# Optimization experiments

Hardware: AMD Instinct MI355X
Metric: run time of the kernel (lower is better)

The kernel has to match this reference:

```python
import jax, jax.numpy as jnp
import numpy as np

EPS = 1e-5
GN_GROUPS = 4  # ConvBlock groupnorm num_groups

def _conv3d(x, w, b):
    # x: [B,C,D,H,W], w: [O,I,3,3,3]
    y = jax.lax.conv_general_dilated(x, w, (1, 1, 1), 'SAME',
                                     dimension_numbers=('NCDHW', 'OIDHW', 'NCDHW'))
    return y + b[None, :, None, None, None]

def _groupnorm(x, gamma, beta):
    b, c, d, h, w = x.shape
    xg = x.reshape(b, GN_GROUPS, c // GN_GROUPS, d, h, w)
    m = xg.mean(axis=(2, 3, 4, 5), keepdims=True)
    v = xg.var(axis=(2, 3, 4, 5), keepdims=True)
    xn = ((xg - m) * jax.lax.rsqrt(v + EPS)).reshape(b, c, d, h, w)
    return xn * gamma[None, :, None, None, None] + beta[None, :, None, None, None]

def setup_inputs() -> dict:
    key = jax.random.key(0)
    ks = jax.random.split(key, 8)
    B, C, D, H, W = 4, 64, 16, 16, 16
    R = 4
    f = lambda k, s: jax.random.normal(k, s, dtype=jnp.float32) * 0.05
    return {
        'x': jax.random.normal(ks[0], (B, C, D, H, W), dtype=jnp.float32),
        'w_i': f(ks[1], (C, C, 3, 3, 3)), 'b_i': jnp.zeros((C,), jnp.float32),
        'gamma_i': jnp.ones((C,), jnp.float32), 'beta_i': jnp.zeros((C,), jnp.float32),
        'w_q': f(ks[2], (C // R, C)), 'b_q': jnp.zeros((C // R,), jnp.float32),
        'w_k': f(ks[3], (C // R, C)), 'b_k': jnp.zeros((C // R,), jnp.float32),
        'w_v': f(ks[4], (C, C)), 'b_v': jnp.zeros((C,), jnp.float32),
        'w_o': f(ks[5], (C, C, 3, 3, 3)), 'b_o': jnp.zeros((C,), jnp.float32),
        'gamma_o': jnp.ones((C,), jnp.float32), 'beta_o': jnp.zeros((C,), jnp.float32),
    }

def reference(x, w_i, b_i, gamma_i, beta_i, w_q, b_q, w_k, b_k, w_v, b_v,
              w_o, b_o, gamma_o, beta_o):
    # i_conv: Conv3d(3x3x3) -> GroupNorm(4) -> ReLU
    x = jax.nn.relu(_groupnorm(_conv3d(x, w_i, b_i), gamma_i, beta_i))
    b, c, d, h, w = x.shape
    n = d * h * w
    xf = x.reshape(b, c, n)
    # spatial attention (groups=1): conv1x1 projections as channel matmuls
    q = jnp.einsum('oc,bcn->bon', w_q, xf) + b_q[None, :, None]   # [b, c/r, n]
    k = jnp.einsum('oc,bcn->bon', w_k, xf) + b_k[None, :, None]   # [b, c/r, n]
    v = jnp.einsum('oc,bcn->bon', w_v, xf) + b_v[None, :, None]   # [b, c,   n]
    A = jax.nn.softmax(jnp.einsum('bqn,bqm->bnm', q, k), axis=-1)  # [b, n, n]
    # ans = bmm(value, A^T): ans[b,c,m] = sum_n v[b,c,n] * A[b,m,n]
    sa = jnp.einsum('bcn,bmn->bcm', v, A).reshape(b, c, d, h, w)
    # channel attention
    Ac = jax.nn.softmax(jnp.einsum('bcn,bdn->bcd', xf, xf), axis=-1)  # [b, c, c]
    ca = jnp.einsum('bcd,bdn->bcn', Ac, xf).reshape(b, c, d, h, w)
    y = x + sa + ca
    # o_conv
    return jax.nn.relu(_groupnorm(_conv3d(y, w_o, b_o), gamma_o, beta_o))
```

## Files before the change

### kernel.cpp

```cpp
#include <hip/hip_runtime.h>

#define OFF_T0  0
#define OFF_SA  1048576
#define OFF_QT  2097152
#define OFF_KT  2359296
#define OFF_VB  2621440
#define OFF_YT  3145728
#define OFF_XB  3670016
#define OFF_AC  4194304
#define OFF_WBI 4210688
#define OFF_WBO 4265984
#define OFF_PT  4321280
#define OFF_PO  4325376
#define OFF_MS  6422528
#define WS_NEED ((size_t)6553600 * 4)

typedef __attribute__((ext_vector_type(8))) short short8v;
typedef __attribute__((ext_vector_type(4))) short short4v;
typedef __attribute__((ext_vector_type(4))) float f32x4;

__device__ __forceinline__ ushort f2bf(float f) {
  union { float f; unsigned u; } v; v.f = f;
  unsigned r = (v.u + 0x7fffu + ((v.u >> 16) & 1u)) >> 16;
  return (ushort)r;
}
__device__ __forceinline__ float bf2f(ushort u) {
  union { unsigned u; float f; } v; v.u = ((unsigned)u) << 16;
  return v.f;
}

__global__ __launch_bounds__(256) void wcvt2_k(const float* __restrict__ wi, const float* __restrict__ wo,
    ushort* __restrict__ wbi, ushort* __restrict__ wbo) {
  int idx = blockIdx.x * 256 + threadIdx.x;
  const float* w = idx < 110592 ? wi : wo;
  ushort* wb = idx < 110592 ? wbi : wbo;
  int j = idx < 110592 ? idx : idx - 110592;
  int ci = j & 63, tap = (j >> 6) % 27, co = j / (64 * 27);
  wb[j] = f2bf(w[(co * 64 + ci) * 27 + tap]);
}

__global__ __launch_bounds__(256) void xcvt_k(const float* __restrict__ x, ushort* __restrict__ xb,
    float* __restrict__ pt) {
  if (blockIdx.x == 0 && threadIdx.x < 64) pt[threadIdx.x] = 0.f;
  __shared__ ushort tl[64 * 72];
  int b = blockIdx.x >> 6;
  int n0 = (blockIdx.x & 63) * 64;
  int t = threadIdx.x;
  int ci = t >> 2, q = t & 3;
  const float* src = x + (size_t)(b * 64 + ci) * 4096 + n0 + q * 16;
  #pragma unroll
  for (int i = 0; i < 4; ++i) {
    float4 v = *reinterpret_cast<const float4*>(src + i * 4);
    tl[(q * 16 + i * 4 + 0) * 72 + ci] = f2bf(v.x);
    tl[(q * 16 + i * 4 + 1) * 72 + ci] = f2bf(v.y);
    tl[(q * 16 + i * 4 + 2) * 72 + ci] = f2bf(v.z);
    tl[(q * 16 + i * 4 + 3) * 72 + ci] = f2bf(v.w);
  }
  __syncthreads();
  int n = t >> 2, qq = t & 3;
  ushort* dst = xb + (size_t)(b * 4096 + n0 + n) * 64 + qq * 16;
  *reinterpret_cast<short8v*>(dst) = *reinterpret_cast<const short8v*>(&tl[n * 72 + qq * 16]);
  *reinterpret_cast<short8v*>(dst + 8) = *reinterpret_cast<const short8v*>(&tl[n * 72 + qq * 16 + 8]);
}

__global__ __launch_bounds__(256) void conv_mfma_k(const ushort* __restrict__ xt,
    const ushort* __restrict__ wb, const float* __restrict__ bias, float* __restrict__ out,
    float* __restrict__ ptg) {
  __shared__ __align__(16) ushort xls[18 * 18 * 64];
  __shared__ float sh_st[16];
  int blk = blockIdx.x;
  int h0 = (blk & 3) * 4;
  int d0 = (blk >> 2) & 15;
  int b  = blk >> 6;
  int tid = threadIdx.x;

  const ushort* xtb = xt + (size_t)b * 4096 * 64;
  for (int u = tid; u < 324; u += 256) {
    int w_s = u % 18;
    int row = u / 18;
    int dz = row / 6, h_s = row - dz * 6;
    int d = d0 + dz - 1, h = h0 + h_s - 1, w = w_s - 1;
    ushort* dst = &xls[(row * 18 + w_s) * 64];
    int swz = w_s & 7;
    if (d >= 0 && d < 16 && h >= 0 && h < 16 && w >= 0 && w < 16) {
      const ushort* src = xtb + (size_t)(d * 256 + h * 16 + w) * 64;
      #pragma unroll
      for (int c = 0; c < 8; ++c)
        *reinterpret_cast<short8v*>(dst + ((c ^ swz) << 3)) =
            *reinterpret_cast<const short8v*>(src + (c << 3));
    } else {
      short8v z = {};
      #pragma unroll
      for (int c = 0; c < 8; ++c)
        *reinterpret_cast<short8v*>(dst + ((c ^ swz) << 3)) = z;
    }
  }
  __syncthreads();

  int wv = tid >> 6, l = tid & 63;
  int wn = wv >> 1, wc = wv & 1;
  int lm = l & 15, lg = l >> 4;

  f32x4 acc[2][2] = {};
  const ushort* wbase0 = wb + (size_t)((wc * 2 + 0) * 16 + lm) * 1728 + lg * 8;
  const ushort* wbase1 = wb + (size_t)((wc * 2 + 1) * 16 + lm) * 1728 + lg * 8;

  #pragma unroll 6
  for (int s = 0; s < 54; ++s) {
    int tap = s >> 1, c0h = s & 1;
    int dz = tap / 9, dyx = tap - dz * 9;
    int dy = dyx / 3, dx = dyx - dy * 3;
    int wrow = lm + dx;
    int chunk = ((c0h * 4 + lg) ^ (wrow & 7)) << 3;
    int r0 = ((dz * 6 + wn * 2 + dy) * 18 + wrow) * 64 + chunk;
    short8v a0 = *reinterpret_cast<const short8v*>(&xls[r0]);
    short8v a1 = *reinterpret_cast<const short8v*>(&xls[r0 + 18 * 64]);
    short8v b0 = *reinterpret_cast<const short8v*>(wbase0 + s * 32);
    short8v b1 = *reinterpret_cast<const short8v*>(wbase1 + s * 32);
    acc[0][0] = __builtin_amdgcn_mfma_f32_16x16x32_bf16(a0, b0, acc[0][0], 0, 0, 0);
    acc[0][1] = __builtin_amdgcn_mfma_f32_16x16x32_bf16(a0, b1, acc[0][1], 0, 0, 0);
    acc[1][0] = __builtin_amdgcn_mfma_f32_16x16x32_bf16(a1, b0, acc[1][0], 0, 0, 0);
    acc[1][1] = __builtin_amdgcn_mfma_f32_16x16x32_bf16(a1, b1, acc[1][1], 0, 0, 0);
  }

  float gs[2], gss[2];
  #pragma unroll
  for (int j = 0; j < 2; ++j) {
    gs[j] = 0.f; gss[j] = 0.f;
    int co = (wc * 2 + j) * 16 + lm;
    float bs = bias[co];
    #pragma unroll
    for (int i = 0; i < 2; ++i) {
      int hh = h0 + wn * 2 + i;
      float4 o;
      o.x = acc[i][j][0] + bs; o.y = acc[i][j][1] + bs;
      o.z = acc[i][j][2] + bs; o.w = acc[i][j][3] + bs;
      gs[j]  += o.x + o.y + o.z + o.w;
      gss[j] = fmaf(o.x, o.x, gss[j]); gss[j] = fmaf(o.y, o.y, gss[j]);
      gss[j] = fmaf(o.z, o.z, gss[j]); gss[j] = fmaf(o.w, o.w, gss[j]);
      *reinterpret_cast<float4*>(&out[(size_t)(b * 64 + co) * 4096 + d0 * 256 + hh * 16 + lg * 4]) = o;
    }
  }
  #pragma unroll
  for (int j = 0; j < 2; ++j) {
    #pragma unroll
    for (int off = 32; off > 0; off >>= 1) {
      gs[j]  += __shfl_xor(gs[j], off);
      gss[j] += __shfl_xor(gss[j], off);
    }
    if (l == 0) { sh_st[wv * 4 + j * 2] = gs[j]; sh_st[wv * 4 + j * 2 + 1] = gss[j]; }
  }
  __syncthreads();
  if (tid < 8) {
    int g = tid >> 1, w2 = tid & 1;
    int wcg = g >> 1, j = g & 1;
    float v = sh_st[wcg * 4 + j * 2 + w2] + sh_st[(wcg + 2) * 4 + j * 2 + w2];
    atomicAdd(&ptg[(b * 4 + g) * 2 + w2], v);
  }
}

__global__ __launch_bounds__(256) void gn_apply_k(const float* __restrict__ t, const float* __restrict__ pt,
    const float* __restrict__ gamma, const float* __restrict__ beta, float* __restrict__ out) {
  int idx = blockIdx.x * 256 + threadIdx.x;
  int c = (idx >> 12) & 63, b = idx >> 18;
  int bg = b * 4 + (c >> 4);
  float s0 = pt[bg * 2], ss0 = pt[bg * 2 + 1];
  float m = s0 * (1.f / 65536.f);
  float r = rsqrtf(ss0 * (1.f / 65536.f) - m * m + 1e-5f);
  float ga = r * gamma[c], bb2 = beta[c] - m * r * gamma[c];
  out[idx] = fmaxf(fmaf(t[idx], ga, bb2), 0.f);
}

__global__ __launch_bounds__(256) void proj_all_k(const float* __restrict__ t0, const float* __restrict__ pt0,
    const float* __restrict__ gamma, const float* __restrict__ beta,
    const float* __restrict__ wq, const float* __restrict__ bq,
    const float* __restrict__ wk, const float* __restrict__ bk,
    const float* __restrict__ wv_, const float* __restrict__ bv,
    ushort* __restrict__ qt, ushort* __restrict__ kt, ushort* __restrict__ vt) {
  __shared__ float xls[64 * 68];
  int b = blockIdx.x >> 6, n0 = (blockIdx.x & 63) * 64;
  int tid = threadIdx.x;
  {
    int ci = tid >> 2, q = tid & 3;
    int bg = b * 4 + (ci >> 4);
    float s0 = pt0[bg * 2], ss0 = pt0[bg * 2 + 1];
    float m = s0 * (1.f / 65536.f);
    float rv = rsqrtf(ss0 * (1.f / 65536.f) - m * m + 1e-5f);
    float ga = rv * gamma[ci], bb2 = beta[ci] - m * rv * gamma[ci];
    const float* src = t0 + (size_t)(b * 64 + ci) * 4096 + n0 + q * 16;
    #pragma unroll
    for (int i = 0; i < 4; ++i) {
      float4 v = *reinterpret_cast<const float4*>(src + i * 4);
      float* d = &xls[ci * 68 + q * 16 + i * 4];
      d[0] = fmaxf(fmaf(v.x, ga, bb2), 0.f);
      d[1] = fmaxf(fmaf(v.y, ga, bb2), 0.f);
      d[2] = fmaxf(fmaf(v.z, ga, bb2), 0.f);
      d[3] = fmaxf(fmaf(v.w, ga, bb2), 0.f);
    }
  }
  __syncthreads();
  int n = tid & 63, og = tid >> 6;
  float xr[64];
  #pragma unroll
  for (int c = 0; c < 64; ++c) xr[c] = xls[c * 68 + n];
  if (og < 2) {
    const float* w  = og == 0 ? wq : wk;
    const float* bb = og == 0 ? bq : bk;
    float scale = og == 0 ? 1.4426950408889634f : 1.0f;
    ushort* outp = og == 0 ? qt : kt;
    union { ushort u[16]; short8v v[2]; } pk;
    #pragma unroll
    for (int o = 0; o < 16; ++o) {
      const float* wr = w + o * 64;
      float acc = bb[o];
      #pragma unroll
      for (int c = 0; c < 64; ++c) acc = fmaf(wr[c], xr[c], acc);
      pk.u[o] = f2bf(acc * scale);
    }
    ushort* dst = outp + (size_t)(b * 4096 + n0 + n) * 32;
    *reinterpret_cast<short8v*>(dst) = pk.v[0];
    *reinterpret_cast<short8v*>(dst + 8) = pk.v[1];
    short8v z = {};
    *reinterpret_cast<short8v*>(dst + 16) = z;
    *reinterpret_cast<short8v*>(dst + 24) = z;
  } else {
    int o0 = (og - 2) * 32;
    #pragma unroll
    for (int o = 0; o < 32; ++o) {
      const float* wr = wv_ + (o0 + o) * 64;
      float acc = bv[o0 + o];
      #pragma unroll
      for (int c = 0; c < 64; ++c) acc = fmaf(wr[c], xr[c], acc);
      vt[(size_t)(b * 64 + o0 + o) * 4096 + n0 + n] = f2bf(acc);
    }
  }
}

#define KP 40
#define VP 72
template<bool SPLIT>
__global__ __launch_bounds__(256) void flash_mfma_k(const ushort* __restrict__ qt,
    const ushort* __restrict__ kt, const ushort* __restrict__ vb, float* __restrict__ sa,
    ushort* __restrict__ pacc, float* __restrict__ pms) {
  __shared__ __align__(16) ushort kls[2][64 * KP];
  __shared__ __align__(16) ushort vls[2][64 * VP];
  __shared__ __align__(16) ushort pls[64 * VP];
  int s, mt, b;
  if (SPLIT) { s = blockIdx.x & 3; mt = (blockIdx.x >> 2) & 63; b = blockIdx.x >> 8; }
  else       { s = 0; mt = blockIdx.x & 63; b = blockIdx.x >> 6; }
  const int NT = SPLIT ? 16 : 64;
  int m0 = mt * 64;
  int kofs = s * 1024;
  int tid = threadIdx.x;
  int w = tid >> 6, l = tid & 63;
  int lm = l & 15, lg = l >> 4;

  short8v qf = *reinterpret_cast<const short8v*>(
      qt + (size_t)(b * 4096 + m0 + w * 16 + lm) * 32 + lg * 8);

  f32x4 acc[4] = {};
  float M = -1e30f, S = 0.f;

  int sr = tid >> 2, sq = tid & 3;
  const ushort* ksrc = kt + (size_t)b * 4096 * 32 + (size_t)kofs * 32 + (size_t)sr * 32 + sq * 8;
  const ushort* vsrc = vb + (size_t)b * 64 * 4096 + (size_t)sr * 4096 + kofs + sq * 16;
  int koff = sr * KP + sq * 8;
  int voff = sr * VP + sq * 16;

  {
    short8v kr = *reinterpret_cast<const short8v*>(ksrc);
    short8v v0 = *reinterpret_cast<const short8v*>(vsrc);
    short8v v1 = *reinterpret_cast<const short8v*>(vsrc + 8);
    *reinterpret_cast<short8v*>(&kls[0][koff]) = kr;
    *reinterpret_cast<short8v*>(&vls[0][voff]) = v0;
    *reinterpret_cast<short8v*>(&vls[0][voff + 8]) = v1;
  }

  ushort* plb = &pls[(w * 16 + lm) * VP];

  #pragma unroll 2
  for (int it = 0; it < NT; ++it) {
    int cur = it & 1;
    int nx = it < NT - 1 ? it + 1 : NT - 1;
    short8v knr = *reinterpret_cast<const short8v*>(ksrc + (size_t)nx * 2048);
    short8v vn0 = *reinterpret_cast<const short8v*>(vsrc + nx * 64);
    short8v vn1 = *reinterpret_cast<const short8v*>(vsrc + nx * 64 + 8);

    __syncthreads();

    const ushort* kb  = &kls[cur][0];
    const ushort* vbk = &vls[cur][0];

    f32x4 sf[4];
    #pragma unroll
    for (int nt = 0; nt < 4; ++nt) {
      short8v kf = *reinterpret_cast<const short8v*>(&kb[(nt * 16 + lm) * KP + lg * 8]);
      f32x4 z = {};
      sf[nt] = __builtin_amdgcn_mfma_f32_16x16x32_bf16(kf, qf, z, 0, 0, 0);
    }

    float tmax = -1e30f;
    #pragma unroll
    for (int nt = 0; nt < 4; ++nt)
      #pragma unroll
      for (int r = 0; r < 4; ++r) tmax = fmaxf(tmax, sf[nt][r]);
    tmax = fmaxf(tmax, __shfl_xor(tmax, 16));
    tmax = fmaxf(tmax, __shfl_xor(tmax, 32));
    if (!__all(tmax <= M)) {
      float Mn = fmaxf(M, tmax);
      float sc = __builtin_amdgcn_exp2f(M - Mn);
      M = Mn;
      S *= sc;
      #pragma unroll
      for (int ct = 0; ct < 4; ++ct)
        #pragma unroll
        for (int r = 0; r < 4; ++r) acc[ct][r] *= sc;
    }
    float tsum = 0.f;
    float p[16];
    #pragma unroll
    for (int nt = 0; nt < 4; ++nt)
      #pragma unroll
      for (int r = 0; r < 4; ++r) {
        float e = __builtin_amdgcn_exp2f(sf[nt][r] - M);
        p[nt * 4 + r] = e;
        tsum += e;
      }
    tsum += __shfl_xor(tsum, 16);
    tsum += __shfl_xor(tsum, 32);
    S += tsum;

    #pragma unroll
    for (int nt = 0; nt < 4; ++nt) {
      unsigned p01, p23;
      asm("v_cvt_pk_bf16_f32 %0, %1, %2" : "=v"(p01) : "v"(p[nt * 4 + 0]), "v"(p[nt * 4 + 1]));
      asm("v_cvt_pk_bf16_f32 %0, %1, %2" : "=v"(p23) : "v"(p[nt * 4 + 2]), "v"(p[nt * 4 + 3]));
      union { unsigned u[2]; short4v v; } pk;
      pk.u[0] = p01; pk.u[1] = p23;
      *reinterpret_cast<short4v*>(plb + nt * 16 + lg * 4) = pk.v;
    }
    asm volatile("s_waitcnt lgkmcnt(0)" ::: "memory");
    __builtin_amdgcn_sched_barrier(0);

    #pragma unroll
    for (int nh = 0; nh < 2; ++nh) {
      short8v pf = *reinterpret_cast<const short8v*>(plb + nh * 32 + lg * 8);
      #pragma unroll
      for (int ct = 0; ct < 4; ++ct) {
        short8v vf = *reinterpret_cast<const short8v*>(&vbk[(ct * 16 + lm) * VP + nh * 32 + lg * 8]);
        acc[ct] = __builtin_amdgcn_mfma_f32_16x16x32_bf16(vf, pf, acc[ct], 0, 0, 0);
      }
    }

    if (it < NT - 1) {
      *reinterpret_cast<short8v*>(&kls[cur ^ 1][koff]) = knr;
      *reinterpret_cast<short8v*>(&vls[cur ^ 1][voff]) = vn0;
      *reinterpret_cast<short8v*>(&vls[cur ^ 1][voff + 8]) = vn1;
    }
  }

  if (SPLIT) {
    int blk = (b * 64 + mt) * 4 + s;
    ushort* pa = pacc + (size_t)blk * 4096;
    #pragma unroll
    for (int ct = 0; ct < 4; ++ct)
      #pragma unroll
      for (int r = 0; r < 4; ++r)
        pa[(ct * 16 + lg * 4 + r) * 64 + w * 16 + lm] = f2bf(acc[ct][r]);
    if (l < 16) {
      pms[(size_t)blk * 128 + (w * 16 + lm) * 2]     = M;
      pms[(size_t)blk * 128 + (w * 16 + lm) * 2 + 1] = S;
    }
  } else {
    float inv = 1.f / S;
    #pragma unroll
    for (int ct = 0; ct < 4; ++ct)
      #pragma unroll
      for (int r = 0; r < 4; ++r)
        sa[(size_t)(b * 64 + ct * 16 + lg * 4 + r) * 4096 + m0 + w * 16 + lm] = acc[ct][r] * inv;
  }
}

__global__ __launch_bounds__(256) void gram_partial_k(const float* __restrict__ t0,
    const float* __restrict__ pt0, const float* __restrict__ gamma, const float* __restrict__ beta,
    float* __restrict__ pg) {
  __shared__ __align__(16) ushort hi[64 * 64];
  __shared__ __align__(16) ushort lo[64 * 64];
  int b = blockIdx.x >> 5, ks = blockIdx.x & 31;
  int tid = threadIdx.x;
  int wv = tid >> 6, l = tid & 63, lm = l & 15, lg = l >> 4;
  int wr = wv >> 1, wd = wv & 1;
  f32x4 acc[2][2] = {};
  int sr = tid >> 2, sq = tid & 3;
  int bg = b * 4 + (sr >> 4);
  float s0p = pt0[bg * 2], ss0p = pt0[bg * 2 + 1];
  float mq = s0p * (1.f / 65536.f);
  float rq = rsqrtf(ss0p * (1.f / 65536.f) - mq * mq + 1e-5f);
  float ga = rq * gamma[sr], bb2 = beta[sr] - mq * rq * gamma[sr];
  const float* xb = t0 + (size_t)b * 262144;

  for (int kt = 0; kt < 2; ++kt) {
    int n0 = ks * 128 + kt * 64;
    __syncthreads();
    const float* src = xb + (size_t)sr * 4096 + n0 + sq * 16;
    #pragma unroll
    for (int c2 = 0; c2 < 2; ++c2) {
      int chunk = sq * 2 + c2;
      int dchunk = chunk ^ (sr & 7);
      short8v hvv, lvv;
      #pragma unroll
      for (int j = 0; j < 8; ++j) {
        float v = fmaxf(fmaf(src[c2 * 8 + j], ga, bb2), 0.f);
        ushort hb = f2bf(v);
        union { float f; unsigned u; } uu; uu.u = ((unsigned)hb) << 16;
        hvv[j] = (short)hb;
        lvv[j] = (short)f2bf(v - uu.f);
      }
      *reinterpret_cast<short8v*>(&hi[sr * 64 + dchunk * 8]) = hvv;
      *reinterpret_cast<short8v*>(&lo[sr * 64 + dchunk * 8]) = lvv;
    }
    __syncthreads();
    #pragma unroll
    for (int kk = 0; kk < 2; ++kk) {
      short8v ah[2], al[2], bh[2], bl[2];
      #pragma unroll
      for (int i = 0; i < 2; ++i) {
        int rc = wr * 32 + i * 16 + lm;
        int ca = ((kk * 4 + lg) ^ (rc & 7)) * 8;
        ah[i] = *reinterpret_cast<const short8v*>(&hi[rc * 64 + ca]);
        al[i] = *reinterpret_cast<const short8v*>(&lo[rc * 64 + ca]);
        int rd = wd * 32 + i * 16 + lm;
        int cb = ((kk * 4 + lg) ^ (rd & 7)) * 8;
        bh[i] = *reinterpret_cast<const short8v*>(&hi[rd * 64 + cb]);
        bl[i] = *reinterpret_cast<const short8v*>(&lo[rd * 64 + cb]);
      }
      #pragma unroll
      for (int i = 0; i < 2; ++i)
        #pragma unroll
        for (int j = 0; j < 2; ++j) {
          acc[i][j] = __builtin_amdgcn_mfma_f32_16x16x32_bf16(ah[i], bh[j], acc[i][j], 0, 0, 0);
          acc[i][j] = __builtin_amdgcn_mfma_f32_16x16x32_bf16(ah[i], bl[j], acc[i][j], 0, 0, 0);
          acc[i][j] = __builtin_amdgcn_mfma_f32_16x16x32_bf16(al[i], bh[j], acc[i][j], 0, 0, 0);
        }
    }
  }
  float* pgb = pg + (size_t)blockIdx.x * 4096;
  #pragma unroll
  for (int i = 0; i < 2; ++i)
    #pragma unroll
    for (int j = 0; j < 2; ++j)
      #pragma unroll
      for (int r = 0; r < 4; ++r) {
        int c = wr * 32 + i * 16 + lg * 4 + r;
        int d = wd * 32 + j * 16 + lm;
        pgb[c * 64 + d] = acc[i][j][r];
      }
}

__global__ __launch_bounds__(256) void gram_softmax_k(const float* __restrict__ pg, float* __restrict__ Ac) {
  int b = blockIdx.x;
  int t = threadIdx.x;
  int r = t >> 2, q = t & 3;
  float4 s[4] = {};
  for (int ks = 0; ks < 32; ++ks) {
    const float* row = pg + ((size_t)(b * 32 + ks) * 64 + r) * 64 + q * 16;
    #pragma unroll
    for (int i = 0; i < 4; ++i) {
      float4 v = *reinterpret_cast<const float4*>(row + i * 4);
      s[i].x += v.x; s[i].y += v.y; s[i].z += v.z; s[i].w += v.w;
    }
  }
  float mx = -1e30f;
  #pragma unroll
  for (int i = 0; i < 4; ++i)
    mx = fmaxf(mx, fmaxf(fmaxf(s[i].x, s[i].y), fmaxf(s[i].z, s[i].w)));
  mx = fmaxf(mx, __shfl_xor(mx, 1));
  mx = fmaxf(mx, __shfl_xor(mx, 2));
  float sum = 0.f;
  #pragma unroll
  for (int i = 0; i < 4; ++i) {
    s[i].x = __expf(s[i].x - mx); s[i].y = __expf(s[i].y - mx);
    s[i].z = __expf(s[i].z - mx); s[i].w = __expf(s[i].w - mx);
    sum += s[i].x + s[i].y + s[i].z + s[i].w;
  }
  sum += __shfl_xor(sum, 1);
  sum += __shfl_xor(sum, 2);
  float inv = 1.f / sum;
  float* dst = Ac + ((size_t)(b * 64 + r)) * 64 + q * 16;
  #pragma unroll
  for (int i = 0; i < 4; ++i) {
    float4 o; o.x = s[i].x * inv; o.y = s[i].y * inv; o.z = s[i].z * inv; o.w = s[i].w * inv;
    *reinterpret_cast<float4*>(dst + i * 4) = o;
  }
}

template<int NSPLIT>
__global__ __launch_bounds__(256) void ca_apply_k(const float* __restrict__ t0,
    const float* __restrict__ pt0, const float* __restrict__ gamma, const float* __restrict__ beta,
    const float* __restrict__ Ac, const float* __restrict__ sa,
    const ushort* __restrict__ pacc, const float* __restrict__ pms, ushort* __restrict__ yt) {
  __shared__ float x1f[64 * 72];
  __shared__ float acf[64 * 72];
  __shared__ float wls[4 * 64];
  int b = blockIdx.x >> 6, mt = blockIdx.x & 63;
  int n0 = mt * 64;
  int tid = threadIdx.x;
  {
    int d = tid >> 2, q = tid & 3;
    int bg = b * 4 + (d >> 4);
    float s0p = pt0[bg * 2], ss0p = pt0[bg * 2 + 1];
    float mq = s0p * (1.f / 65536.f);
    float rq = rsqrtf(ss0p * (1.f / 65536.f) - mq * mq + 1e-5f);
    float ga = rq * gamma[d], bb2 = beta[d] - mq * rq * gamma[d];
    const float* xs = t0 + (size_t)(b * 64 + d) * 4096 + n0 + q * 16;
    const float* as = Ac + (size_t)(b * 64 + d) * 64 + q * 16;
    #pragma unroll
    for (int i = 0; i < 4; ++i) {
      float4 v = *reinterpret_cast<const float4*>(xs + i * 4);
      x1f[d * 72 + q * 16 + i * 4 + 0] = fmaxf(fmaf(v.x, ga, bb2), 0.f);
      x1f[d * 72 + q * 16 + i * 4 + 1] = fmaxf(fmaf(v.y, ga, bb2), 0.f);
      x1f[d * 72 + q * 16 + i * 4 + 2] = fmaxf(fmaf(v.z, ga, bb2), 0.f);
      x1f[d * 72 + q * 16 + i * 4 + 3] = fmaxf(fmaf(v.w, ga, bb2), 0.f);
      float4 a = *reinterpret_cast<const float4*>(as + i * 4);
      acf[d * 72 + q * 16 + i * 4 + 0] = a.x;
      acf[d * 72 + q * 16 + i * 4 + 1] = a.y;
      acf[d * 72 + q * 16 + i * 4 + 2] = a.z;
      acf[d * 72 + q * 16 + i * 4 + 3] = a.w;
    }
  }
  if (NSPLIT > 1 && tid < 64) {
    int m = tid;
    size_t msb = (size_t)(b * 64 + mt) * NSPLIT * 128;
    float Ms[NSPLIT], Ss[NSPLIT];
    float Mg = -1e30f;
    #pragma unroll
    for (int s = 0; s < NSPLIT; ++s) {
      Ms[s] = pms[msb + s * 128 + m * 2];
      Ss[s] = pms[msb + s * 128 + m * 2 + 1];
      Mg = fmaxf(Mg, Ms[s]);
    }
    float Stot = 0.f;
    #pragma unroll
    for (int s = 0; s < NSPLIT; ++s) {
      float wv = __builtin_amdgcn_exp2f(Ms[s] - Mg);
      wls[s * 64 + m] = wv;
      Stot += wv * Ss[s];
    }
    float inv = 1.f / Stot;
    #pragma unroll
    for (int s = 0; s < NSPLIT; ++s) wls[s * 64 + m] *= inv;
  }
  __syncthreads();
  int m = tid & 63, cg = tid >> 6;
  float sval[16];
  if (NSPLIT > 1) {
    #pragma unroll
    for (int ci = 0; ci < 16; ++ci) sval[ci] = 0.f;
    const ushort* pb = pacc + (size_t)(b * 64 + mt) * NSPLIT * 4096;
    #pragma unroll
    for (int s = 0; s < NSPLIT; ++s) {
      float wv = wls[s * 64 + m];
      #pragma unroll
      for (int ci = 0; ci < 16; ++ci)
        sval[ci] = fmaf(wv, bf2f(pb[s * 4096 + (cg * 16 + ci) * 64 + m]), sval[ci]);
    }
  } else {
    #pragma unroll
    for (int ci = 0; ci < 16; ++ci)
      sval[ci] = sa[(size_t)(b * 64 + cg * 16 + ci) * 4096 + n0 + m];
  }
  float xcol[64];
  #pragma unroll
  for (int d = 0; d < 64; ++d) xcol[d] = x1f[d * 72 + m];
  union { ushort u[16]; short8v v[2]; } pk;
  #pragma unroll
  for (int ci = 0; ci < 16; ++ci) {
    int c = cg * 16 + ci;
    float o = xcol[c] + sval[ci];
    const float* ar = &acf[c * 72];
    #pragma unroll
    for (int d4 = 0; d4 < 16; ++d4) {
      float4 a4 = *reinterpret_cast<const float4*>(ar + d4 * 4);
      o = fmaf(a4.x, xcol[d4 * 4 + 0], o);
      o = fmaf(a4.y, xcol[d4 * 4 + 1], o);
      o = fmaf(a4.z, xcol[d4 * 4 + 2], o);
      o = fmaf(a4.w, xcol[d4 * 4 + 3], o);
    }
    pk.u[ci] = f2bf(o);
  }
  ushort* dst = yt + (size_t)(b * 4096 + n0 + m) * 64 + cg * 16;
  *reinterpret_cast<short8v*>(dst) = pk.v[0];
  *reinterpret_cast<short8v*>(dst + 8) = pk.v[1];
}

extern "C" void kernel_launch(void* const* d_in, const int* in_sizes, int n_in,
                              void* d_out, int out_size, void* d_ws, size_t ws_size,
                              hipStream_t stream) {
  const float* x       = (const float*)d_in[0];
  const float* w_i     = (const float*)d_in[1];
  const float* b_i     = (const float*)d_in[2];
  const float* gamma_i = (const float*)d_in[3];
  const float* beta_i  = (const float*)d_in[4];
  const float* w_q     = (const float*)d_in[5];
  const float* b_q     = (const float*)d_in[6];
  const float* w_k     = (const float*)d_in[7];
  const float* b_k     = (const float*)d_in[8];
  const float* w_v     = (const float*)d_in[9];
  const float* b_v     = (const float*)d_in[10];
  const float* w_o     = (const float*)d_in[11];
  const float* b_o     = (const float*)d_in[12];
  const float* gamma_o = (const float*)d_in[13];
  const float* beta_o  = (const float*)d_in[14];
  float* ws = (float*)d_ws;
  float* t0 = ws + OFF_T0;
  ushort* qt  = (ushort*)(ws + OFF_QT);
  ushort* kt  = (ushort*)(ws + OFF_KT);
  ushort* vbp = (ushort*)(ws + OFF_VB);
  float* yb = ws + OFF_SA;
  float* pg = ws + OFF_QT;
  ushort* ytp = (ushort*)(ws + OFF_YT);
  ushort* xbp = (ushort*)(ws + OFF_XB);
  float* ac = ws + OFF_AC;
  ushort* wbi = (ushort*)(ws + OFF_WBI);
  ushort* wbo = (ushort*)(ws + OFF_WBO);
  float* pt0 = ws + OFF_PT;
  float* pt1 = pt0 + 32;
  ushort* pacc = (ushort*)(ws + OFF_PO);
  float* pms  = ws + OFF_MS;
  float* outp = (float*)d_out;
  bool split = ws_size >= WS_NEED;

  wcvt2_k<<<864, 256, 0, stream>>>(w_i, w_o, wbi, wbo);
  xcvt_k<<<256, 256, 0, stream>>>(x, xbp, pt0);

  conv_mfma_k<<<256, 256, 0, stream>>>(xbp, wbi, b_i, t0, pt0);

  proj_all_k<<<256, 256, 0, stream>>>(t0, pt0, gamma_i, beta_i,
                                      w_q, b_q, w_k, b_k, w_v, b_v, qt, kt, vbp);

  if (split)
    flash_mfma_k<true><<<1024, 256, 0, stream>>>(qt, kt, vbp, yb, pacc, pms);
  else
    flash_mfma_k<false><<<256, 256, 0, stream>>>(qt, kt, vbp, yb, pacc, pms);

  gram_partial_k<<<128, 256, 0, stream>>>(t0, pt0, gamma_i, beta_i, pg);
  gram_softmax_k<<<4, 256, 0, stream>>>(pg, ac);

  if (split)
    ca_apply_k<4><<<256, 256, 0, stream>>>(t0, pt0, gamma_i, beta_i, ac, yb, pacc, pms, ytp);
  else
    ca_apply_k<1><<<256, 256, 0, stream>>>(t0, pt0, gamma_i, beta_i, ac, yb, pacc, pms, ytp);

  conv_mfma_k<<<256, 256, 0, stream>>>(ytp, wbo, b_o, t0, pt1);
  gn_apply_k<<<4096, 256, 0, stream>>>(t0, pt1, gamma_o, beta_o, outp);
}
```

Baseline: 138.4 us.

## Fuse conversion kernels, merge gram into projection, move channel softmax into apply

```diff
diff --git a/kernel.cpp b/kernel.cpp
--- a/kernel.cpp
+++ b/kernel.cpp
@@ -28,39 +28,46 @@
   union { unsigned u; float f; } v; v.u = ((unsigned)u) << 16;
   return v.f;
 }
-
-__global__ __launch_bounds__(256) void wcvt2_k(const float* __restrict__ wi, const float* __restrict__ wo,
-    ushort* __restrict__ wbi, ushort* __restrict__ wbo) {
-  int idx = blockIdx.x * 256 + threadIdx.x;
-  const float* w = idx < 110592 ? wi : wo;
-  ushort* wb = idx < 110592 ? wbi : wbo;
-  int j = idx < 110592 ? idx : idx - 110592;
-  int ci = j & 63, tap = (j >> 6) % 27, co = j / (64 * 27);
-  wb[j] = f2bf(w[(co * 64 + ci) * 27 + tap]);
-}
-
-__global__ __launch_bounds__(256) void xcvt_k(const float* __restrict__ x, ushort* __restrict__ xb,
-    float* __restrict__ pt) {
-  if (blockIdx.x == 0 && threadIdx.x < 64) pt[threadIdx.x] = 0.f;
+__device__ __forceinline__ float max3f(float a, float b, float c) {
+  return fmaxf(fmaxf(a, b), c);
+}
+
+__global__ __launch_bounds__(256) void cvt_k(const float* __restrict__ x, ushort* __restrict__ xb,
+    float* __restrict__ pt, const float* __restrict__ wi, const float* __restrict__ wo,
+    ushort* __restrict__ wbi, ushort* __restrict__ wbo, float* __restrict__ acr) {
   __shared__ ushort tl[64 * 72];
-  int b = blockIdx.x >> 6;
-  int n0 = (blockIdx.x & 63) * 64;
+  int blk = blockIdx.x;
   int t = threadIdx.x;
-  int ci = t >> 2, q = t & 3;
-  const float* src = x + (size_t)(b * 64 + ci) * 4096 + n0 + q * 16;
-  #pragma unroll
-  for (int i = 0; i < 4; ++i) {
-    float4 v = *reinterpret_cast<const float4*>(src + i * 4);
-    tl[(q * 16 + i * 4 + 0) * 72 + ci] = f2bf(v.x);
-    tl[(q * 16 + i * 4 + 1) * 72 + ci] = f2bf(v.y);
-    tl[(q * 16 + i * 4 + 2) * 72 + ci] = f2bf(v.z);
-    tl[(q * 16 + i * 4 + 3) * 72 + ci] = f2bf(v.w);
-  }
-  __syncthreads();
-  int n = t >> 2, qq = t & 3;
-  ushort* dst = xb + (size_t)(b * 4096 + n0 + n) * 64 + qq * 16;
-  *reinterpret_cast<short8v*>(dst) = *reinterpret_cast<const short8v*>(&tl[n * 72 + qq * 16]);
-  *reinterpret_cast<short8v*>(dst + 8) = *reinterpret_cast<const short8v*>(&tl[n * 72 + qq * 16 + 8]);
+  if (blk < 256) {
+    int b = blk >> 6;
+    int n0 = (blk & 63) * 64;
+    int ci = t >> 2, q = t & 3;
+    const float* src = x + (size_t)(b * 64 + ci) * 4096 + n0 + q * 16;
+    #pragma unroll
+    for (int i = 0; i < 4; ++i) {
+      float4 v = *reinterpret_cast<const float4*>(src + i * 4);
+      tl[(q * 16 + i * 4 + 0) * 72 + ci] = f2bf(v.x);
+      tl[(q * 16 + i * 4 + 1) * 72 + ci] = f2bf(v.y);
+      tl[(q * 16 + i * 4 + 2) * 72 + ci] = f2bf(v.z);
+      tl[(q * 16 + i * 4 + 3) * 72 + ci] = f2bf(v.w);
+    }
+    __syncthreads();
+    int n = t >> 2, qq = t & 3;
+    ushort* dst = xb + (size_t)(b * 4096 + n0 + n) * 64 + qq * 16;
+    *reinterpret_cast<short8v*>(dst) = *reinterpret_cast<const short8v*>(&tl[n * 72 + qq * 16]);
+    *reinterpret_cast<short8v*>(dst + 8) = *reinterpret_cast<const short8v*>(&tl[n * 72 + qq * 16 + 8]);
+  } else if (blk < 1120) {
+    int idx = (blk - 256) * 256 + t;
+    const float* w = idx < 110592 ? wi : wo;
+    ushort* wb = idx < 110592 ? wbi : wbo;
+    int j = idx < 110592 ? idx : idx - 110592;
+    int ci = j & 63, tap = (j >> 6) % 27, co = j / (64 * 27);
+    wb[j] = f2bf(w[(co * 64 + ci) * 27 + tap]);
+  } else {
+    int idx = (blk - 1120) * 256 + t;
+    acr[idx] = 0.f;
+    if (blk == 1120 && t < 64) pt[t] = 0.f;
+  }
 }
 
 __global__ __launch_bounds__(256) void conv_mfma_k(const ushort* __restrict__ xt,
@@ -171,68 +178,145 @@
   out[idx] = fmaxf(fmaf(t[idx], ga, bb2), 0.f);
 }
 
-__global__ __launch_bounds__(256) void proj_all_k(const float* __restrict__ t0, const float* __restrict__ pt0,
+__global__ __launch_bounds__(256) void projgram_k(const float* __restrict__ t0, const float* __restrict__ pt0,
     const float* __restrict__ gamma, const float* __restrict__ beta,
     const float* __restrict__ wq, const float* __restrict__ bq,
     const float* __restrict__ wk, const float* __restrict__ bk,
     const float* __restrict__ wv_, const float* __restrict__ bv,
-    ushort* __restrict__ qt, ushort* __restrict__ kt, ushort* __restrict__ vt) {
-  __shared__ float xls[64 * 68];
-  int b = blockIdx.x >> 6, n0 = (blockIdx.x & 63) * 64;
+    ushort* __restrict__ qt, ushort* __restrict__ kt, ushort* __restrict__ vt,
+    float* __restrict__ acr) {
+  __shared__ __align__(16) float smem[64 * 68];
+  int blk = blockIdx.x;
   int tid = threadIdx.x;
-  {
-    int ci = tid >> 2, q = tid & 3;
-    int bg = b * 4 + (ci >> 4);
-    float s0 = pt0[bg * 2], ss0 = pt0[bg * 2 + 1];
-    float m = s0 * (1.f / 65536.f);
-    float rv = rsqrtf(ss0 * (1.f / 65536.f) - m * m + 1e-5f);
-    float ga = rv * gamma[ci], bb2 = beta[ci] - m * rv * gamma[ci];
-    const float* src = t0 + (size_t)(b * 64 + ci) * 4096 + n0 + q * 16;
-    #pragma unroll
-    for (int i = 0; i < 4; ++i) {
-      float4 v = *reinterpret_cast<const float4*>(src + i * 4);
-      float* d = &xls[ci * 68 + q * 16 + i * 4];
-      d[0] = fmaxf(fmaf(v.x, ga, bb2), 0.f);
-      d[1] = fmaxf(fmaf(v.y, ga, bb2), 0.f);
-      d[2] = fmaxf(fmaf(v.z, ga, bb2), 0.f);
-      d[3] = fmaxf(fmaf(v.w, ga, bb2), 0.f);
-    }
-  }
-  __syncthreads();
-  int n = tid & 63, og = tid >> 6;
-  float xr[64];
-  #pragma unroll
-  for (int c = 0; c < 64; ++c) xr[c] = xls[c * 68 + n];
-  if (og < 2) {
-    const float* w  = og == 0 ? wq : wk;
-    const float* bb = og == 0 ? bq : bk;
-    float scale = og == 0 ? 1.4426950408889634f : 1.0f;
-    ushort* outp = og == 0 ? qt : kt;
-    union { ushort u[16]; short8v v[2]; } pk;
-    #pragma unroll
-    for (int o = 0; o < 16; ++o) {
-      const float* wr = w + o * 64;
-      float acc = bb[o];
-      #pragma unroll
-      for (int c = 0; c < 64; ++c) acc = fmaf(wr[c], xr[c], acc);
-      pk.u[o] = f2bf(acc * scale);
-    }
-    ushort* dst = outp + (size_t)(b * 4096 + n0 + n) * 32;
-    *reinterpret_cast<short8v*>(dst) = pk.v[0];
-    *reinterpret_cast<short8v*>(dst + 8) = pk.v[1];
-    short8v z = {};
-    *reinterpret_cast<short8v*>(dst + 16) = z;
-    *reinterpret_cast<short8v*>(dst + 24) = z;
+  if (blk < 256) {
+    float* xls = smem;
+    int b = blk >> 6, n0 = (blk & 63) * 64;
+    {
+      int ci = tid >> 2, q = tid & 3;
+      int bg = b * 4 + (ci >> 4);
+      float s0 = pt0[bg * 2], ss0 = pt0[bg * 2 + 1];
+      float m = s0 * (1.f / 65536.f);
+      float rv = rsqrtf(ss0 * (1.f / 65536.f) - m * m + 1e-5f);
+      float ga = rv * gamma[ci], bb2 = beta[ci] - m * rv * gamma[ci];
+      const float* src = t0 + (size_t)(b * 64 + ci) * 4096 + n0 + q * 16;
+      #pragma unroll
+      for (int i = 0; i < 4; ++i) {
+        float4 v = *reinterpret_cast<const float4*>(src + i * 4);
+        float* d = &xls[ci * 68 + q * 16 + i * 4];
+        d[0] = fmaxf(fmaf(v.x, ga, bb2), 0.f);
+        d[1] = fmaxf(fmaf(v.y, ga, bb2), 0.f);
+        d[2] = fmaxf(fmaf(v.z, ga, bb2), 0.f);
+        d[3] = fmaxf(fmaf(v.w, ga, bb2), 0.f);
+      }
+    }
+    __syncthreads();
+    int n = tid & 63, og = tid >> 6;
+    float xr[64];
+    #pragma unroll
+    for (int c = 0; c < 64; ++c) xr[c] = xls[c * 68 + n];
+    if (og < 2) {
+      const float* w  = og == 0 ? wq : wk;
+      const float* bb = og == 0 ? bq : bk;
+      float scale = og == 0 ? 1.4426950408889634f : 1.0f;
+      ushort* outp = og == 0 ? qt : kt;
+      union { ushort u[16]; short8v v[2]; } pk;
+      #pragma unroll
+      for (int o = 0; o < 16; ++o) {
+        const float* wr = w + o * 64;
+        float acc = bb[o];
+        #pragma unroll
+        for (int c = 0; c < 64; ++c) acc = fmaf(wr[c], xr[c], acc);
+        pk.u[o] = f2bf(acc * scale);
+      }
+      ushort* dst = outp + (size_t)(b * 4096 + n0 + n) * 32;
+      *reinterpret_cast<short8v*>(dst) = pk.v[0];
+      *reinterpret_cast<short8v*>(dst + 8) = pk.v[1];
+      short8v z = {};
+      *reinterpret_cast<short8v*>(dst + 16) = z;
+      *reinterpret_cast<short8v*>(dst + 24) = z;
+    } else {
+      int o0 = (og - 2) * 32;
+      #pragma unroll
+      for (int o = 0; o < 32; ++o) {
+        const float* wr = wv_ + (o0 + o) * 64;
+        float acc = bv[o0 + o];
+        #pragma unroll
+        for (int c = 0; c < 64; ++c) acc = fmaf(wr[c], xr[c], acc);
+        vt[(size_t)(b * 64 + o0 + o) * 4096 + n0 + n] = f2bf(acc);
+      }
+    }
   } else {
-    int o0 = (og - 2) * 32;
-    #pragma unroll
-    for (int o = 0; o < 32; ++o) {
-      const float* wr = wv_ + (o0 + o) * 64;
-      float acc = bv[o0 + o];
-      #pragma unroll
-      for (int c = 0; c < 64; ++c) acc = fmaf(wr[c], xr[c], acc);
-      vt[(size_t)(b * 64 + o0 + o) * 4096 + n0 + n] = f2bf(acc);
-    }
+    ushort* hi = (ushort*)smem;
+    ushort* lo = hi + 4096;
+    int gblk = blk - 256;
+    int b = gblk >> 5, ks = gblk & 31;
+    int wv = tid >> 6, l = tid & 63, lm = l & 15, lg = l >> 4;
+    int wr = wv >> 1, wd = wv & 1;
+    f32x4 acc[2][2] = {};
+    int sr = tid >> 2, sq = tid & 3;
+    int bg = b * 4 + (sr >> 4);
+    float s0p = pt0[bg * 2], ss0p = pt0[bg * 2 + 1];
+    float mq = s0p * (1.f / 65536.f);
+    float rq = rsqrtf(ss0p * (1.f / 65536.f) - mq * mq + 1e-5f);
+    float ga = rq * gamma[sr], bb2 = beta[sr] - mq * rq * gamma[sr];
+    const float* xb = t0 + (size_t)b * 262144;
+
+    for (int kt2 = 0; kt2 < 2; ++kt2) {
+      int n0 = ks * 128 + kt2 * 64;
+      __syncthreads();
+      const float* src = xb + (size_t)sr * 4096 + n0 + sq * 16;
+      #pragma unroll
+      for (int c2 = 0; c2 < 2; ++c2) {
+        int chunk = sq * 2 + c2;
+        int dchunk = chunk ^ (sr & 7);
+        short8v hvv, lvv;
+        #pragma unroll
+        for (int j = 0; j < 8; ++j) {
+          float v = fmaxf(fmaf(src[c2 * 8 + j], ga, bb2), 0.f);
+          ushort hb = f2bf(v);
+          union { float f; unsigned u; } uu; uu.u = ((unsigned)hb) << 16;
+          hvv[j] = (short)hb;
+          lvv[j] = (short)f2bf(v - uu.f);
+        }
+        *reinterpret_cast<short8v*>(hi + sr * 64 + dchunk * 8) = hvv;
+        *reinterpret_cast<short8v*>(lo + sr * 64 + dchunk * 8) = lvv;
+      }
+      __syncthreads();
+      #pragma unroll
+      for (int kk = 0; kk < 2; ++kk) {
+        short8v ah[2], al[2], bh[2], bl[2];
+        #pragma unroll
+        for (int i = 0; i < 2; ++i) {
+          int rc = wr * 32 + i * 16 + lm;
+          int ca = ((kk * 4 + lg) ^ (rc & 7)) * 8;
+          ah[i] = *reinterpret_cast<const short8v*>(hi + rc * 64 + ca);
+          al[i] = *reinterpret_cast<const short8v*>(lo + rc * 64 + ca);
+          int rd = wd * 32 + i * 16 + lm;
+          int cb = ((kk * 4 + lg) ^ (rd & 7)) * 8;
+          bh[i] = *reinterpret_cast<const short8v*>(hi + rd * 64 + cb);
+          bl[i] = *reinterpret_cast<const short8v*>(lo + rd * 64 + cb);
+        }
+        #pragma unroll
+        for (int i = 0; i < 2; ++i)
+          #pragma unroll
+          for (int j = 0; j < 2; ++j) {
+            acc[i][j] = __builtin_amdgcn_mfma_f32_16x16x32_bf16(ah[i], bh[j], acc[i][j], 0, 0, 0);
+            acc[i][j] = __builtin_amdgcn_mfma_f32_16x16x32_bf16(ah[i], bl[j], acc[i][j], 0, 0, 0);
+            acc[i][j] = __builtin_amdgcn_mfma_f32_16x16x32_bf16(al[i], bh[j], acc[i][j], 0, 0, 0);
+          }
+      }
+    }
+    float* acb = acr + (size_t)b * 4096;
+    #pragma unroll
+    for (int i = 0; i < 2; ++i)
+      #pragma unroll
+      for (int j = 0; j < 2; ++j)
+        #pragma unroll
+        for (int r = 0; r < 4; ++r) {
+          int c = wr * 32 + i * 16 + lg * 4 + r;
+          int d = wd * 32 + j * 16 + lm;
+          atomicAdd(&acb[c * 64 + d], acc[i][j][r]);
+        }
   }
 }
 
@@ -299,11 +383,12 @@
       sf[nt] = __builtin_amdgcn_mfma_f32_16x16x32_bf16(kf, qf, z, 0, 0, 0);
     }
 
-    float tmax = -1e30f;
-    #pragma unroll
-    for (int nt = 0; nt < 4; ++nt)
-      #pragma unroll
-      for (int r = 0; r < 4; ++r) tmax = fmaxf(tmax, sf[nt][r]);
+    float t0_ = max3f(sf[0][0], sf[0][1], sf[0][2]);
+    float t1_ = max3f(sf[0][3], sf[1][0], sf[1][1]);
+    float t2_ = max3f(sf[1][2], sf[1][3], sf[2][0]);
+    float t3_ = max3f(sf[2][1], sf[2][2], sf[2][3]);
+    float t4_ = max3f(sf[3][0], sf[3][1], sf[3][2]);
+    float tmax = fmaxf(max3f(t0_, t1_, t2_), max3f(t3_, t4_, sf[3][3]));
     tmax = fmaxf(tmax, __shfl_xor(tmax, 16));
     tmax = fmaxf(tmax, __shfl_xor(tmax, 32));
     if (!__all(tmax <= M)) {
@@ -360,16 +445,16 @@
   }
 
   if (SPLIT) {
-    int blk = (b * 64 + mt) * 4 + s;
-    ushort* pa = pacc + (size_t)blk * 4096;
+    int blk2 = (b * 64 + mt) * 4 + s;
+    ushort* pa = pacc + (size_t)blk2 * 4096;
     #pragma unroll
     for (int ct = 0; ct < 4; ++ct)
       #pragma unroll
       for (int r = 0; r < 4; ++r)
         pa[(ct * 16 + lg * 4 + r) * 64 + w * 16 + lm] = f2bf(acc[ct][r]);
     if (l < 16) {
-      pms[(size_t)blk * 128 + (w * 16 + lm) * 2]     = M;
-      pms[(size_t)blk * 128 + (w * 16 + lm) * 2 + 1] = S;
+      pms[(size_t)blk2 * 128 + (w * 16 + lm) * 2]     = M;
+      pms[(size_t)blk2 * 128 + (w * 16 + lm) * 2 + 1] = S;
     }
   } else {
     float inv = 1.f / S;
@@ -378,126 +463,13 @@
       #pragma unroll
       for (int r = 0; r < 4; ++r)
         sa[(size_t)(b * 64 + ct * 16 + lg * 4 + r) * 4096 + m0 + w * 16 + lm] = acc[ct][r] * inv;
-  }
-}
-
-__global__ __launch_bounds__(256) void gram_partial_k(const float* __restrict__ t0,
-    const float* __restrict__ pt0, const float* __restrict__ gamma, const float* __restrict__ beta,
-    float* __restrict__ pg) {
-  __shared__ __align__(16) ushort hi[64 * 64];
-  __shared__ __align__(16) ushort lo[64 * 64];
-  int b = blockIdx.x >> 5, ks = blockIdx.x & 31;
-  int tid = threadIdx.x;
-  int wv = tid >> 6, l = tid & 63, lm = l & 15, lg = l >> 4;
-  int wr = wv >> 1, wd = wv & 1;
-  f32x4 acc[2][2] = {};
-  int sr = tid >> 2, sq = tid & 3;
-  int bg = b * 4 + (sr >> 4);
-  float s0p = pt0[bg * 2], ss0p = pt0[bg * 2 + 1];
-  float mq = s0p * (1.f / 65536.f);
-  float rq = rsqrtf(ss0p * (1.f / 65536.f) - mq * mq + 1e-5f);
-  float ga = rq * gamma[sr], bb2 = beta[sr] - mq * rq * gamma[sr];
-  const float* xb = t0 + (size_t)b * 262144;
-
-  for (int kt = 0; kt < 2; ++kt) {
-    int n0 = ks * 128 + kt * 64;
-    __syncthreads();
-    const float* src = xb + (size_t)sr * 4096 + n0 + sq * 16;
-    #pragma unroll
-    for (int c2 = 0; c2 < 2; ++c2) {
-      int chunk = sq * 2 + c2;
-      int dchunk = chunk ^ (sr & 7);
-      short8v hvv, lvv;
-      #pragma unroll
-      for (int j = 0; j < 8; ++j) {
-        float v = fmaxf(fmaf(src[c2 * 8 + j], ga, bb2), 0.f);
-        ushort hb = f2bf(v);
-        union { float f; unsigned u; } uu; uu.u = ((unsigned)hb) << 16;
-        hvv[j] = (short)hb;
-        lvv[j] = (short)f2bf(v - uu.f);
-      }
-      *reinterpret_cast<short8v*>(&hi[sr * 64 + dchunk * 8]) = hvv;
-      *reinterpret_cast<short8v*>(&lo[sr * 64 + dchunk * 8]) = lvv;
-    }
-    __syncthreads();
-    #pragma unroll
-    for (int kk = 0; kk < 2; ++kk) {
-      short8v ah[2], al[2], bh[2], bl[2];
-      #pragma unroll
-      for (int i = 0; i < 2; ++i) {
-        int rc = wr * 32 + i * 16 + lm;
-        int ca = ((kk * 4 + lg) ^ (rc & 7)) * 8;
-        ah[i] = *reinterpret_cast<const short8v*>(&hi[rc * 64 + ca]);
-        al[i] = *reinterpret_cast<const short8v*>(&lo[rc * 64 + ca]);
-        int rd = wd * 32 + i * 16 + lm;
-        int cb = ((kk * 4 + lg) ^ (rd & 7)) * 8;
-        bh[i] = *reinterpret_cast<const short8v*>(&hi[rd * 64 + cb]);
-        bl[i] = *reinterpret_cast<const short8v*>(&lo[rd * 64 + cb]);
-      }
-      #pragma unroll
-      for (int i = 0; i < 2; ++i)
-        #pragma unroll
-        for (int j = 0; j < 2; ++j) {
-          acc[i][j] = __builtin_amdgcn_mfma_f32_16x16x32_bf16(ah[i], bh[j], acc[i][j], 0, 0, 0);
-          acc[i][j] = __builtin_amdgcn_mfma_f32_16x16x32_bf16(ah[i], bl[j], acc[i][j], 0, 0, 0);
-          acc[i][j] = __builtin_amdgcn_mfma_f32_16x16x32_bf16(al[i], bh[j], acc[i][j], 0, 0, 0);
-        }
-    }
-  }
-  float* pgb = pg + (size_t)blockIdx.x * 4096;
-  #pragma unroll
-  for (int i = 0; i < 2; ++i)
-    #pragma unroll
-    for (int j = 0; j < 2; ++j)
-      #pragma unroll
-      for (int r = 0; r < 4; ++r) {
-        int c = wr * 32 + i * 16 + lg * 4 + r;
-        int d = wd * 32 + j * 16 + lm;
-        pgb[c * 64 + d] = acc[i][j][r];
-      }
-}
-
-__global__ __launch_bounds__(256) void gram_softmax_k(const float* __restrict__ pg, float* __restrict__ Ac) {
-  int b = blockIdx.x;
-  int t = threadIdx.x;
-  int r = t >> 2, q = t & 3;
-  float4 s[4] = {};
-  for (int ks = 0; ks < 32; ++ks) {
-    const float* row = pg + ((size_t)(b * 32 + ks) * 64 + r) * 64 + q * 16;
-    #pragma unroll
-    for (int i = 0; i < 4; ++i) {
-      float4 v = *reinterpret_cast<const float4*>(row + i * 4);
-      s[i].x += v.x; s[i].y += v.y; s[i].z += v.z; s[i].w += v.w;
-    }
-  }
-  float mx = -1e30f;
-  #pragma unroll
-  for (int i = 0; i < 4; ++i)
-    mx = fmaxf(mx, fmaxf(fmaxf(s[i].x, s[i].y), fmaxf(s[i].z, s[i].w)));
-  mx = fmaxf(mx, __shfl_xor(mx, 1));
-  mx = fmaxf(mx, __shfl_xor(mx, 2));
-  float sum = 0.f;
-  #pragma unroll
-  for (int i = 0; i < 4; ++i) {
-    s[i].x = __expf(s[i].x - mx); s[i].y = __expf(s[i].y - mx);
-    s[i].z = __expf(s[i].z - mx); s[i].w = __expf(s[i].w - mx);
-    sum += s[i].x + s[i].y + s[i].z + s[i].w;
-  }
-  sum += __shfl_xor(sum, 1);
-  sum += __shfl_xor(sum, 2);
-  float inv = 1.f / sum;
-  float* dst = Ac + ((size_t)(b * 64 + r)) * 64 + q * 16;
-  #pragma unroll
-  for (int i = 0; i < 4; ++i) {
-    float4 o; o.x = s[i].x * inv; o.y = s[i].y * inv; o.z = s[i].z * inv; o.w = s[i].w * inv;
-    *reinterpret_cast<float4*>(dst + i * 4) = o;
   }
 }
 
 template<int NSPLIT>
 __global__ __launch_bounds__(256) void ca_apply_k(const float* __restrict__ t0,
     const float* __restrict__ pt0, const float* __restrict__ gamma, const float* __restrict__ beta,
-    const float* __restrict__ Ac, const float* __restrict__ sa,
+    const float* __restrict__ acr, const float* __restrict__ sa,
     const ushort* __restrict__ pacc, const float* __restrict__ pms, ushort* __restrict__ yt) {
   __shared__ float x1f[64 * 72];
   __shared__ float acf[64 * 72];
@@ -513,7 +485,7 @@
     float rq = rsqrtf(ss0p * (1.f / 65536.f) - mq * mq + 1e-5f);
     float ga = rq * gamma[d], bb2 = beta[d] - mq * rq * gamma[d];
     const float* xs = t0 + (size_t)(b * 64 + d) * 4096 + n0 + q * 16;
-    const float* as = Ac + (size_t)(b * 64 + d) * 64 + q * 16;
+    const float* as = acr + (size_t)(b * 64 + d) * 64 + q * 16;
     #pragma unroll
     for (int i = 0; i < 4; ++i) {
       float4 v = *reinterpret_cast<const float4*>(xs + i * 4);
@@ -549,6 +521,25 @@
     float inv = 1.f / Stot;
     #pragma unroll
     for (int s = 0; s < NSPLIT; ++s) wls[s * 64 + m] *= inv;
+  }
+  __syncthreads();
+  {
+    int r = tid >> 2, q4 = tid & 3;
+    float* row = &acf[r * 72 + q4 * 16];
+    float mx = -1e30f;
+    #pragma unroll
+    for (int i = 0; i < 16; ++i) mx = fmaxf(mx, row[i]);
+    mx = fmaxf(mx, __shfl_xor(mx, 1));
+    mx = fmaxf(mx, __shfl_xor(mx, 2));
+    float e[16];
+    float sum = 0.f;
+    #pragma unroll
+    for (int i = 0; i < 16; ++i) { e[i] = __expf(row[i] - mx); sum += e[i]; }
+    sum += __shfl_xor(sum, 1);
+    sum += __shfl_xor(sum, 2);
+    float inv = 1.f / sum;
+    #pragma unroll
+    for (int i = 0; i < 16; ++i) row[i] = e[i] * inv;
   }
   __syncthreads();
   int m = tid & 63, cg = tid >> 6;
@@ -617,10 +608,9 @@
   ushort* kt  = (ushort*)(ws + OFF_KT);
   ushort* vbp = (ushort*)(ws + OFF_VB);
   float* yb = ws + OFF_SA;
-  float* pg = ws + OFF_QT;
   ushort* ytp = (ushort*)(ws + OFF_YT);
   ushort* xbp = (ushort*)(ws + OFF_XB);
-  float* ac = ws + OFF_AC;
+  float* acr = ws + OFF_AC;
   ushort* wbi = (ushort*)(ws + OFF_WBI);
   ushort* wbo = (ushort*)(ws + OFF_WBO);
   float* pt0 = ws + OFF_PT;
@@ -630,26 +620,22 @@
   float* outp = (float*)d_out;
   bool split = ws_size >= WS_NEED;
 
-  wcvt2_k<<<864, 256, 0, stream>>>(w_i, w_o, wbi, wbo);
-  xcvt_k<<<256, 256, 0, stream>>>(x, xbp, pt0);
+  cvt_k<<<1184, 256, 0, stream>>>(x, xbp, pt0, w_i, w_o, wbi, wbo, acr);
 
   conv_mfma_k<<<256, 256, 0, stream>>>(xbp, wbi, b_i, t0, pt0);
 
-  proj_all_k<<<256, 256, 0, stream>>>(t0, pt0, gamma_i, beta_i,
-                                      w_q, b_q, w_k, b_k, w_v, b_v, qt, kt, vbp);
+  projgram_k<<<384, 256, 0, stream>>>(t0, pt0, gamma_i, beta_i,
+                                      w_q, b_q, w_k, b_k, w_v, b_v, qt, kt, vbp, acr);
 
   if (split)
     flash_mfma_k<true><<<1024, 256, 0, stream>>>(qt, kt, vbp, yb, pacc, pms);
   else
     flash_mfma_k<false><<<256, 256, 0, stream>>>(qt, kt, vbp, yb, pacc, pms);
 
-  gram_partial_k<<<128, 256, 0, stream>>>(t0, pt0, gamma_i, beta_i, pg);
-  gram_softmax_k<<<4, 256, 0, stream>>>(pg, ac);
-
   if (split)
-    ca_apply_k<4><<<256, 256, 0, stream>>>(t0, pt0, gamma_i, beta_i, ac, yb, pacc, pms, ytp);
+    ca_apply_k<4><<<256, 256, 0, stream>>>(t0, pt0, gamma_i, beta_i, acr, yb, pacc, pms, ytp);
   else
-    ca_apply_k<1><<<256, 256, 0, stream>>>(t0, pt0, gamma_i, beta_i, ac, yb, pacc, pms, ytp);
+    ca_apply_k<1><<<256, 256, 0, stream>>>(t0, pt0, gamma_i, beta_i, acr, yb, pacc, pms, ytp);
 
   conv_mfma_k<<<256, 256, 0, stream>>>(ytp, wbo, b_o, t0, pt1);
   gn_apply_k<<<4096, 256, 0, stream>>>(t0, pt1, gamma_o, beta_o, outp);
```

Measured after the change: 119.7 us. -13.5%, faster.
